# Performance work log

Hardware: AMD Instinct MI355X
Metric: run time of the kernel (lower is better)

## Reference

```python
import jax, jax.numpy as jnp
import numpy as np
import math

M = 0.5
S = 30.0
COS_M = math.cos(M)
SIN_M = math.sin(M)


def setup_inputs() -> dict:
    key = jax.random.key(0)
    k1, k2, k3 = jax.random.split(key, 3)
    batch, din, nclass = 512, 512, 100000
    x = jax.random.normal(k1, (batch, din), dtype=jnp.float32)
    # xavier_uniform for weight (out, in)
    limit = math.sqrt(6.0 / (nclass + din))
    w = jax.random.uniform(k2, (nclass, din), dtype=jnp.float32, minval=-limit, maxval=limit)
    target = jax.random.randint(k3, (batch,), 0, nclass, dtype=jnp.int64)
    return {"input": x, "weight": w, "target": target}


def reference(input, weight, target):
    # L2-normalize rows (torch F.normalize uses eps=1e-12 clamp on norm)
    xn = input / jnp.maximum(jnp.linalg.norm(input, axis=1, keepdims=True), 1e-12)
    wn = weight / jnp.maximum(jnp.linalg.norm(weight, axis=1, keepdims=True), 1e-12)
    cosine = xn @ wn.T  # [B, C]
    sine = jnp.sqrt(jnp.maximum(1.0 - cosine * cosine, 0.0))
    phi = cosine * COS_M - sine * SIN_M
    # easy_margin=True
    phi = jnp.where(cosine > 0, phi, cosine)
    one_hot = jax.nn.one_hot(target, cosine.shape[1], dtype=cosine.dtype)  # [B, C]
    logits = S * (one_hot * phi + (1.0 - one_hot) * cosine)
    # cross-entropy with mean reduction
    logp = jax.nn.log_softmax(logits, axis=1)
    nll = -jnp.take_along_axis(logp, target[:, None], axis=1)[:, 0]
    return jnp.mean(nll)
```

## Files before the change

### kernel.cpp

```cpp
#include <hip/hip_runtime.h>
#include <math.h>

#define BATCH 512
#define DIM 512
#define NCLASS 100000
#define BN 64
#define NBLK ((NCLASS + BN - 1) / BN)
#define S_SCALE 30.0f
#define COSM 0.8775825618903728f
#define SINM 0.4794255386042030f

typedef unsigned short u16;
typedef __attribute__((ext_vector_type(8))) short short8;
typedef __attribute__((ext_vector_type(4))) float floatx4;


__device__ __forceinline__ u16 f2bf(float f) {
    union { float f; unsigned int u; } v;
    v.f = f;
    unsigned int u = v.u;
    u += 0x7fffu + ((u >> 16) & 1u);
    return (u16)(u >> 16);
}

__global__ void xnorm_kernel(const float* __restrict__ x, u16* __restrict__ xn) {
    const int row = blockIdx.x;
    const int t = threadIdx.x;
    const floatx4* xr = (const floatx4*)(x + (size_t)row * DIM);
    floatx4 a = xr[t];
    floatx4 b = xr[t + 64];
    float ss = a[0]*a[0] + a[1]*a[1] + a[2]*a[2] + a[3]*a[3]
             + b[0]*b[0] + b[1]*b[1] + b[2]*b[2] + b[3]*b[3];
#pragma unroll
    for (int d = 1; d < 64; d <<= 1) ss += __shfl_xor(ss, d);
    const float rn = 1.0f / fmaxf(sqrtf(ss), 1e-12f);
    ushort4 ua, ub;
    ua.x = f2bf(a[0]*rn); ua.y = f2bf(a[1]*rn); ua.z = f2bf(a[2]*rn); ua.w = f2bf(a[3]*rn);
    ub.x = f2bf(b[0]*rn); ub.y = f2bf(b[1]*rn); ub.z = f2bf(b[2]*rn); ub.w = f2bf(b[3]*rn);
    u16* orow = xn + (size_t)row * DIM;
    *(ushort4*)(orow + 4*t)       = ua;
    *(ushort4*)(orow + 256 + 4*t) = ub;
}

__global__ void arcface_main(const float* __restrict__ w,
                             const u16* __restrict__ xn,
                             const int* __restrict__ target,
                             float* __restrict__ partials,
                             float* __restrict__ tlogit) {
    __shared__ u16 wb[BN * DIM];

    const int c0 = blockIdx.x * BN;
    const int t = threadIdx.x;

    {
        const int r = t >> 3;
        const int q = t & 7;
        const int cg = c0 + r;
        floatx4 v[16];
        float ss = 0.f;
        if (cg < NCLASS) {
            const floatx4* wr = (const floatx4*)(w + (size_t)cg * DIM);
#pragma unroll
            for (int i = 0; i < 16; ++i) {
                v[i] = wr[q + (i << 3)];
                ss += v[i][0]*v[i][0] + v[i][1]*v[i][1] + v[i][2]*v[i][2] + v[i][3]*v[i][3];
            }
        } else {
#pragma unroll
            for (int i = 0; i < 16; ++i) { v[i][0]=0.f; v[i][1]=0.f; v[i][2]=0.f; v[i][3]=0.f; }
        }
        ss += __shfl_xor(ss, 1);
        ss += __shfl_xor(ss, 2);
        ss += __shfl_xor(ss, 4);
        const float rs = 1.0f / fmaxf(sqrtf(ss), 1e-12f);
#pragma unroll
        for (int i = 0; i < 16; ++i) {
            const int col4 = q + (i << 3);
            const int gp = (col4 >> 1) ^ (r & 7);
            const int off = r * DIM + gp * 8 + (col4 & 1) * 4;
            ushort4 u;
            u.x = f2bf(v[i][0] * rs); u.y = f2bf(v[i][1] * rs);
            u.z = f2bf(v[i][2] * rs); u.w = f2bf(v[i][3] * rs);
            *(ushort4*)(&wb[off]) = u;
        }
    }
    __syncthreads();

    const int wave = t >> 6;
    const int lane = t & 63;
    const int quad = lane >> 4;
    const int nin  = lane & 15;
    const int mbase = wave * 64;

    floatx4 acc[4][4];
#pragma unroll
    for (int mi = 0; mi < 4; ++mi)
#pragma unroll
        for (int ni = 0; ni < 4; ++ni) {
            acc[mi][ni][0] = 0.f; acc[mi][ni][1] = 0.f;
            acc[mi][ni][2] = 0.f; acc[mi][ni][3] = 0.f;
        }

    for (int kk = 0; kk < 16; ++kk) {
        short8 a[4], b[4];
        const int k = kk * 32 + quad * 8;
#pragma unroll
        for (int mi = 0; mi < 4; ++mi) {
            const int m = mbase + mi * 16 + nin;
            a[mi] = *(const short8*)(xn + (size_t)m * DIM + k);
        }
#pragma unroll
        for (int ni = 0; ni < 4; ++ni) {
            const int cl = ni * 16 + nin;
            const int gp = ((kk << 2) + quad) ^ (cl & 7);
            b[ni] = *(const short8*)(&wb[cl * DIM + gp * 8]);
        }
#pragma unroll
        for (int mi = 0; mi < 4; ++mi)
#pragma unroll
            for (int ni = 0; ni < 4; ++ni)
                acc[mi][ni] = __builtin_amdgcn_mfma_f32_16x16x32_bf16(
                    a[mi], b[ni], acc[mi][ni], 0, 0, 0);
    }

#pragma unroll
    for (int mi = 0; mi < 4; ++mi) {
#pragma unroll
        for (int reg = 0; reg < 4; ++reg) {
            const int m = mbase + mi * 16 + quad * 4 + reg;
            const int tg = target[m];
            float psum = 0.f;
#pragma unroll
            for (int ni = 0; ni < 4; ++ni) {
                const int c = c0 + ni * 16 + nin;
                if (c < NCLASS) {
                    const float cosv = acc[mi][ni][reg];
                    float lg;
                    if (c == tg) {
                        const float sine = sqrtf(fmaxf(1.f - cosv * cosv, 0.f));
                        float phi = cosv * COSM - sine * SINM;
                        if (!(cosv > 0.f)) phi = cosv;
                        lg = S_SCALE * phi;
                        tlogit[m] = lg;
                    } else {
                        lg = S_SCALE * cosv;
                    }
                    psum += __expf(lg - S_SCALE);
                }
            }
            psum += __shfl_xor(psum, 1);
            psum += __shfl_xor(psum, 2);
            psum += __shfl_xor(psum, 4);
            psum += __shfl_xor(psum, 8);
            if (nin == 0)
                partials[(size_t)blockIdx.x * BATCH + m] = psum;
        }
    }
}

__global__ void reduce_lse(const float* __restrict__ partials,
                           const float* __restrict__ tlogit,
                           float* __restrict__ nll) {
    const int m = blockIdx.x;
    const int t = threadIdx.x;
    float s = 0.f;
    for (int b = t; b < NBLK; b += 256) s += partials[(size_t)b * BATCH + m];
#pragma unroll
    for (int d = 1; d < 64; d <<= 1) s += __shfl_xor(s, d);
    __shared__ float red[4];
    if ((t & 63) == 0) red[t >> 6] = s;
    __syncthreads();
    if (t == 0) {
        const float tot = red[0] + red[1] + red[2] + red[3];
        nll[m] = (logf(tot) + S_SCALE) - tlogit[m];
    }
}

__global__ void reduce_mean(const float* __restrict__ nll, float* __restrict__ out) {
    const int t = threadIdx.x;
    float s = nll[t];
#pragma unroll
    for (int d = 1; d < 64; d <<= 1) s += __shfl_xor(s, d);
    __shared__ float red[8];
    if ((t & 63) == 0) red[t >> 6] = s;
    __syncthreads();
    if (t == 0) {
        float tot = 0.f;
#pragma unroll
        for (int i = 0; i < 8; ++i) tot += red[i];
        out[0] = tot / (float)BATCH;
    }
}

extern "C" void kernel_launch(void* const* d_in, const int* in_sizes, int n_in,
                              void* d_out, int out_size, void* d_ws, size_t ws_size,
                              hipStream_t stream) {
    const float* x = (const float*)d_in[0];
    const float* w = (const float*)d_in[1];
    const int* target = (const int*)d_in[2];

    char* ws = (char*)d_ws;
    u16* xn        = (u16*)ws;
    float* tlogit  = (float*)(ws + 524288);
    float* nll     = (float*)(ws + 526336);
    float* partials= (float*)(ws + 528384);

    xnorm_kernel<<<BATCH, 64, 0, stream>>>(x, xn);
    arcface_main<<<NBLK, 512, 0, stream>>>(w, xn, target, partials, tlogit);
    reduce_lse<<<BATCH, 256, 0, stream>>>(partials, tlogit, nll);
    reduce_mean<<<1, 512, 0, stream>>>(nll, (float*)d_out);
}
```

Before: 402.4 us.

## Make main kernel persistent with double-buffered weight tiles and prefetch overlap

The main kernel now launches a fixed grid of 256 blocks that loop over class tiles. Each iteration loads the next tile's weights into registers during the MFMA loop and writes them into a second shared-memory buffer afterwards, so global loads overlap compute. The weight-norm scaling is applied to the accumulator instead of before bf16 conversion, targets are held in registers, and partials are stored row-major so the reduction reads contiguously. In exchange, register pressure is higher and LDS use doubles, which may limit occupancy, and rounding changes slightly because unnormalized weights are converted to bf16.

```diff
diff --git a/kernel.cpp b/kernel.cpp
--- a/kernel.cpp
+++ b/kernel.cpp
@@ -6,6 +6,7 @@
 #define NCLASS 100000
 #define BN 64
 #define NBLK ((NCLASS + BN - 1) / BN)
+#define GRID 256
 #define S_SCALE 30.0f
 #define COSM 0.8775825618903728f
 #define SINM 0.4794255386042030f
@@ -42,55 +43,43 @@
     *(ushort4*)(orow + 256 + 4*t) = ub;
 }
 
-__global__ void arcface_main(const float* __restrict__ w,
-                             const u16* __restrict__ xn,
-                             const int* __restrict__ target,
-                             float* __restrict__ partials,
-                             float* __restrict__ tlogit) {
-    __shared__ u16 wb[BN * DIM];
-
-    const int c0 = blockIdx.x * BN;
-    const int t = threadIdx.x;
-
-    {
-        const int r = t >> 3;
-        const int q = t & 7;
-        const int cg = c0 + r;
-        floatx4 v[16];
-        float ss = 0.f;
-        if (cg < NCLASS) {
-            const floatx4* wr = (const floatx4*)(w + (size_t)cg * DIM);
-#pragma unroll
-            for (int i = 0; i < 16; ++i) {
-                v[i] = wr[q + (i << 3)];
-                ss += v[i][0]*v[i][0] + v[i][1]*v[i][1] + v[i][2]*v[i][2] + v[i][3]*v[i][3];
-            }
-        } else {
-#pragma unroll
-            for (int i = 0; i < 16; ++i) { v[i][0]=0.f; v[i][1]=0.f; v[i][2]=0.f; v[i][3]=0.f; }
-        }
-        ss += __shfl_xor(ss, 1);
-        ss += __shfl_xor(ss, 2);
-        ss += __shfl_xor(ss, 4);
-        const float rs = 1.0f / fmaxf(sqrtf(ss), 1e-12f);
-#pragma unroll
-        for (int i = 0; i < 16; ++i) {
-            const int col4 = q + (i << 3);
-            const int gp = (col4 >> 1) ^ (r & 7);
-            const int off = r * DIM + gp * 8 + (col4 & 1) * 4;
-            ushort4 u;
-            u.x = f2bf(v[i][0] * rs); u.y = f2bf(v[i][1] * rs);
-            u.z = f2bf(v[i][2] * rs); u.w = f2bf(v[i][3] * rs);
-            *(ushort4*)(&wb[off]) = u;
-        }
-    }
-    __syncthreads();
-
-    const int wave = t >> 6;
-    const int lane = t & 63;
-    const int quad = lane >> 4;
-    const int nin  = lane & 15;
-    const int mbase = wave * 64;
+__device__ __forceinline__ void stage_write(const floatx4* v, u16* __restrict__ wbuf,
+                                            float* __restrict__ rsbuf, int sr, int sq) {
+    float ss = 0.f;
+#pragma unroll
+    for (int i = 0; i < 16; ++i)
+        ss += v[i][0]*v[i][0] + v[i][1]*v[i][1] + v[i][2]*v[i][2] + v[i][3]*v[i][3];
+    ss += __shfl_xor(ss, 1);
+    ss += __shfl_xor(ss, 2);
+    ss += __shfl_xor(ss, 4);
+    if (sq == 0) rsbuf[sr] = 1.0f / fmaxf(sqrtf(ss), 1e-12f);
+#pragma unroll
+    for (int i = 0; i < 16; ++i) {
+        const int col4 = sq + (i << 3);
+        const int gp = (col4 >> 1) ^ (sr & 7);
+        const int off = sr * DIM + gp * 8 + (col4 & 1) * 4;
+        ushort4 u;
+        u.x = f2bf(v[i][0]); u.y = f2bf(v[i][1]);
+        u.z = f2bf(v[i][2]); u.w = f2bf(v[i][3]);
+        *(ushort4*)(&wbuf[off]) = u;
+    }
+}
+
+template<bool PREF>
+__device__ __forceinline__ void process_tile(
+        const float* __restrict__ w, const u16* __restrict__ xn,
+        float* __restrict__ partials, float* __restrict__ tlogit,
+        const u16* __restrict__ wbc, u16* __restrict__ wbn,
+        const float* __restrict__ rsc, float* __restrict__ rsn,
+        const int* __restrict__ tgt, int tile,
+        int mbase, int quad, int nin, int sr, int sq) {
+
+    floatx4 v[16];
+    const floatx4* wr = (const floatx4*)w;
+    if (PREF) {
+        const int cg = min((tile + GRID) * BN + sr, NCLASS - 1);
+        wr = (const floatx4*)(w + (size_t)cg * DIM);
+    }
 
     floatx4 acc[4][4];
 #pragma unroll
@@ -101,19 +90,20 @@
             acc[mi][ni][2] = 0.f; acc[mi][ni][3] = 0.f;
         }
 
+    const u16* xbase = xn + (size_t)(mbase + nin) * DIM + quad * 8;
+
+#pragma unroll
     for (int kk = 0; kk < 16; ++kk) {
+        if (PREF) v[kk] = wr[sq + (kk << 3)];
         short8 a[4], b[4];
-        const int k = kk * 32 + quad * 8;
-#pragma unroll
-        for (int mi = 0; mi < 4; ++mi) {
-            const int m = mbase + mi * 16 + nin;
-            a[mi] = *(const short8*)(xn + (size_t)m * DIM + k);
-        }
+#pragma unroll
+        for (int mi = 0; mi < 4; ++mi)
+            a[mi] = *(const short8*)(xbase + (size_t)mi * 16 * DIM + kk * 32);
 #pragma unroll
         for (int ni = 0; ni < 4; ++ni) {
             const int cl = ni * 16 + nin;
             const int gp = ((kk << 2) + quad) ^ (cl & 7);
-            b[ni] = *(const short8*)(&wb[cl * DIM + gp * 8]);
+            b[ni] = *(const short8*)(&wbc[cl * DIM + gp * 8]);
         }
 #pragma unroll
         for (int mi = 0; mi < 4; ++mi)
@@ -123,18 +113,23 @@
                     a[mi], b[ni], acc[mi][ni], 0, 0, 0);
     }
 
+    const int c0 = tile * BN;
+    float rsl[4];
+#pragma unroll
+    for (int ni = 0; ni < 4; ++ni) rsl[ni] = rsc[ni * 16 + nin];
+
 #pragma unroll
     for (int mi = 0; mi < 4; ++mi) {
 #pragma unroll
         for (int reg = 0; reg < 4; ++reg) {
             const int m = mbase + mi * 16 + quad * 4 + reg;
-            const int tg = target[m];
+            const int tg = tgt[mi * 4 + reg];
             float psum = 0.f;
 #pragma unroll
             for (int ni = 0; ni < 4; ++ni) {
                 const int c = c0 + ni * 16 + nin;
                 if (c < NCLASS) {
-                    const float cosv = acc[mi][ni][reg];
+                    const float cosv = acc[mi][ni][reg] * rsl[ni];
                     float lg;
                     if (c == tg) {
                         const float sine = sqrtf(fmaxf(1.f - cosv * cosv, 0.f));
@@ -153,9 +148,59 @@
             psum += __shfl_xor(psum, 4);
             psum += __shfl_xor(psum, 8);
             if (nin == 0)
-                partials[(size_t)blockIdx.x * BATCH + m] = psum;
+                partials[(size_t)m * NBLK + tile] = psum;
         }
     }
+
+    if (PREF) stage_write(v, wbn, rsn, sr, sq);
+}
+
+__global__ __launch_bounds__(512, 2) void arcface_main(
+        const float* __restrict__ w, const u16* __restrict__ xn,
+        const int* __restrict__ target, float* __restrict__ partials,
+        float* __restrict__ tlogit) {
+    __shared__ __align__(16) u16 wb[2][BN * DIM];
+    __shared__ float rs_s[2][BN];
+
+    const int t = threadIdx.x;
+    const int wave = t >> 6;
+    const int lane = t & 63;
+    const int quad = lane >> 4;
+    const int nin  = lane & 15;
+    const int mbase = wave * 64;
+    const int sr = t >> 3;
+    const int sq = t & 7;
+
+    int tgt[16];
+#pragma unroll
+    for (int mi = 0; mi < 4; ++mi)
+#pragma unroll
+        for (int reg = 0; reg < 4; ++reg)
+            tgt[mi * 4 + reg] = target[mbase + mi * 16 + quad * 4 + reg];
+
+    {
+        const int cg = min((int)blockIdx.x * BN + sr, NCLASS - 1);
+        const floatx4* wr = (const floatx4*)(w + (size_t)cg * DIM);
+        floatx4 v[16];
+#pragma unroll
+        for (int i = 0; i < 16; ++i) v[i] = wr[sq + (i << 3)];
+        stage_write(v, wb[0], rs_s[0], sr, sq);
+    }
+    __syncthreads();
+
+    int cur = 0;
+    int tile = blockIdx.x;
+    while (tile + GRID < NBLK) {
+        process_tile<true>(w, xn, partials, tlogit,
+                           wb[cur], wb[cur ^ 1], rs_s[cur], rs_s[cur ^ 1],
+                           tgt, tile, mbase, quad, nin, sr, sq);
+        __syncthreads();
+        cur ^= 1;
+        tile += GRID;
+    }
+    process_tile<false>(w, xn, partials, tlogit,
+                        wb[cur], wb[cur ^ 1], rs_s[cur], rs_s[cur ^ 1],
+                        tgt, tile, mbase, quad, nin, sr, sq);
 }
 
 __global__ void reduce_lse(const float* __restrict__ partials,
@@ -163,8 +208,9 @@
                            float* __restrict__ nll) {
     const int m = blockIdx.x;
     const int t = threadIdx.x;
+    const float* row = partials + (size_t)m * NBLK;
     float s = 0.f;
-    for (int b = t; b < NBLK; b += 256) s += partials[(size_t)b * BATCH + m];
+    for (int b = t; b < NBLK; b += 256) s += row[b];
 #pragma unroll
     for (int d = 1; d < 64; d <<= 1) s += __shfl_xor(s, d);
     __shared__ float red[4];
@@ -206,7 +252,7 @@
     float* partials= (float*)(ws + 528384);
 
     xnorm_kernel<<<BATCH, 64, 0, stream>>>(x, xn);
-    arcface_main<<<NBLK, 512, 0, stream>>>(w, xn, target, partials, tlogit);
+    arcface_main<<<GRID, 512, 0, stream>>>(w, xn, target, partials, tlogit);
     reduce_lse<<<BATCH, 256, 0, stream>>>(partials, tlogit, nll);
     reduce_mean<<<1, 512, 0, stream>>>(nll, (float*)d_out);
 }
```

Result: slower. 573.6 us (+42.5%).

## Restructure ArcFace GEMM as persistent tiles with normalization folded into epilogue

Applied to the files above, without the earlier changes.

Replaces the one-block-per-64-classes kernel with a persistent 256-block grid. Each block holds a 128-row slice of normalized x in shared memory and streams 256-class weight tiles straight from global memory into registers. Weights are converted to bf16 in registers without normalizing, and the row norm is applied as a scale in the exp2 epilogue. The MFMA shape moves to 32x32x16. The target-logit margin is moved to reduce_lse, which recomputes the target cosine and swaps its exp term into the sum. This removes the shared-memory staging of W and shrinks the partials array, but adds recomputation and a dependency on reading x in bf16.

```diff
diff --git a/kernel.cpp b/kernel.cpp
--- a/kernel.cpp
+++ b/kernel.cpp
@@ -1,26 +1,34 @@
 #include <hip/hip_runtime.h>
+#include <hip/hip_bf16.h>
 #include <math.h>
 
 #define BATCH 512
 #define DIM 512
 #define NCLASS 100000
-#define BN 64
-#define NBLK ((NCLASS + BN - 1) / BN)
+#define BNB 256
+#define NT 391
+#define NSTREAM 64
+#define GRID 256
 #define S_SCALE 30.0f
 #define COSM 0.8775825618903728f
 #define SINM 0.4794255386042030f
+#define LOG2E 1.44269504088896f
 
 typedef unsigned short u16;
 typedef __attribute__((ext_vector_type(8))) short short8;
 typedef __attribute__((ext_vector_type(4))) float floatx4;
+typedef __attribute__((ext_vector_type(16))) float floatx16;
 
 
 __device__ __forceinline__ u16 f2bf(float f) {
+    union { __hip_bfloat16 h; u16 u; } c;
+    c.h = __float2bfloat16(f);
+    return c.u;
+}
+__device__ __forceinline__ float bf2f(u16 b) {
     union { float f; unsigned int u; } v;
-    v.f = f;
-    unsigned int u = v.u;
-    u += 0x7fffu + ((u >> 16) & 1u);
-    return (u16)(u >> 16);
+    v.u = ((unsigned int)b) << 16;
+    return v.f;
 }
 
 __global__ void xnorm_kernel(const float* __restrict__ x, u16* __restrict__ xn) {
@@ -42,137 +50,186 @@
     *(ushort4*)(orow + 256 + 4*t) = ub;
 }
 
-__global__ void arcface_main(const float* __restrict__ w,
-                             const u16* __restrict__ xn,
-                             const int* __restrict__ target,
-                             float* __restrict__ partials,
-                             float* __restrict__ tlogit) {
-    __shared__ u16 wb[BN * DIM];
-
-    const int c0 = blockIdx.x * BN;
-    const int t = threadIdx.x;
+__device__ __forceinline__ short8 cvt_bf8(floatx4 a, floatx4 b) {
+    union { short8 s8; u16 u[8]; } p;
+#pragma unroll
+    for (int j = 0; j < 4; ++j) p.u[j] = f2bf(a[j]);
+#pragma unroll
+    for (int j = 0; j < 4; ++j) p.u[4 + j] = f2bf(b[j]);
+    return p.s8;
+}
+
+__global__ __launch_bounds__(512, 1) void arcface_main(
+        const float* __restrict__ w, const u16* __restrict__ xn,
+        float* __restrict__ partials) {
+    __shared__ __align__(16) u16 ash[128 * 512];
+    __shared__ float pacc[8][64];
+
+    const int t = threadIdx.x;
+    const int bid = blockIdx.x;
+    const int stream = bid & 63;
+    const int mgrp = bid >> 6;
+    const int wv = t >> 6;
+    const int lane = t & 63;
+    const int l31 = lane & 31;
+    const int hi = lane >> 5;
+    const int mhalf = wv & 1;
+    const int nslot = wv >> 1;
 
     {
-        const int r = t >> 3;
-        const int q = t & 7;
-        const int cg = c0 + r;
-        floatx4 v[16];
-        float ss = 0.f;
-        if (cg < NCLASS) {
-            const floatx4* wr = (const floatx4*)(w + (size_t)cg * DIM);
-#pragma unroll
-            for (int i = 0; i < 16; ++i) {
-                v[i] = wr[q + (i << 3)];
-                ss += v[i][0]*v[i][0] + v[i][1]*v[i][1] + v[i][2]*v[i][2] + v[i][3]*v[i][3];
+        const u16* xbase = xn + (size_t)(mgrp * 128) * DIM;
+#pragma unroll
+        for (int i = 0; i < 16; ++i) {
+            const int gid = t + i * 512;
+            const int row = gid >> 6;
+            const int g = gid & 63;
+            floatx4 v = *(const floatx4*)(xbase + (size_t)row * DIM + g * 8);
+            *(floatx4*)(&ash[row * DIM + ((g ^ (row & 7)) * 8)]) = v;
+        }
+    }
+    __syncthreads();
+
+    float run[2][16];
+#pragma unroll
+    for (int mf = 0; mf < 2; ++mf)
+#pragma unroll
+        for (int r = 0; r < 16; ++r) run[mf][r] = 0.f;
+
+    const int arow0 = (mhalf * 64 + l31) * DIM;
+    const int arow1 = (mhalf * 64 + 32 + l31) * DIM;
+
+    for (int tile = stream; tile < NT; tile += NSTREAM) {
+        const int c0 = tile * BNB + nslot * 64;
+        bool vfrag[2];
+        const float* wp[2];
+#pragma unroll
+        for (int ni = 0; ni < 2; ++ni) {
+            const int c = c0 + ni * 32 + l31;
+            vfrag[ni] = (c0 + ni * 32) < NCLASS;
+            const int cc = min(c, NCLASS - 1);
+            wp[ni] = w + (size_t)cc * DIM + hi * 8;
+        }
+
+        floatx16 acc[2][2];
+#pragma unroll
+        for (int mf = 0; mf < 2; ++mf)
+#pragma unroll
+            for (int ni = 0; ni < 2; ++ni) acc[mf][ni] = (floatx16)0.0f;
+
+        float ssq[2] = {0.f, 0.f};
+        floatx4 pb[2][2][2];
+#pragma unroll
+        for (int ni = 0; ni < 2; ++ni) {
+            pb[0][ni][0] = *(const floatx4*)(wp[ni]);
+            pb[0][ni][1] = *(const floatx4*)(wp[ni] + 4);
+            pb[1][ni][0] = *(const floatx4*)(wp[ni] + 16);
+            pb[1][ni][1] = *(const floatx4*)(wp[ni] + 20);
+        }
+
+#pragma unroll
+        for (int ks = 0; ks < 32; ++ks) {
+            const int sl = ks & 1;
+            short8 bfr[2];
+#pragma unroll
+            for (int ni = 0; ni < 2; ++ni) {
+                floatx4 lo = pb[sl][ni][0], hp = pb[sl][ni][1];
+                ssq[ni] += lo[0]*lo[0] + lo[1]*lo[1] + lo[2]*lo[2] + lo[3]*lo[3]
+                         + hp[0]*hp[0] + hp[1]*hp[1] + hp[2]*hp[2] + hp[3]*hp[3];
+                bfr[ni] = cvt_bf8(lo, hp);
             }
-        } else {
-#pragma unroll
-            for (int i = 0; i < 16; ++i) { v[i][0]=0.f; v[i][1]=0.f; v[i][2]=0.f; v[i][3]=0.f; }
-        }
-        ss += __shfl_xor(ss, 1);
-        ss += __shfl_xor(ss, 2);
-        ss += __shfl_xor(ss, 4);
-        const float rs = 1.0f / fmaxf(sqrtf(ss), 1e-12f);
-#pragma unroll
-        for (int i = 0; i < 16; ++i) {
-            const int col4 = q + (i << 3);
-            const int gp = (col4 >> 1) ^ (r & 7);
-            const int off = r * DIM + gp * 8 + (col4 & 1) * 4;
-            ushort4 u;
-            u.x = f2bf(v[i][0] * rs); u.y = f2bf(v[i][1] * rs);
-            u.z = f2bf(v[i][2] * rs); u.w = f2bf(v[i][3] * rs);
-            *(ushort4*)(&wb[off]) = u;
-        }
-    }
-    __syncthreads();
-
-    const int wave = t >> 6;
-    const int lane = t & 63;
-    const int quad = lane >> 4;
-    const int nin  = lane & 15;
-    const int mbase = wave * 64;
-
-    floatx4 acc[4][4];
-#pragma unroll
-    for (int mi = 0; mi < 4; ++mi)
-#pragma unroll
-        for (int ni = 0; ni < 4; ++ni) {
-            acc[mi][ni][0] = 0.f; acc[mi][ni][1] = 0.f;
-            acc[mi][ni][2] = 0.f; acc[mi][ni][3] = 0.f;
-        }
-
-    for (int kk = 0; kk < 16; ++kk) {
-        short8 a[4], b[4];
-        const int k = kk * 32 + quad * 8;
-#pragma unroll
-        for (int mi = 0; mi < 4; ++mi) {
-            const int m = mbase + mi * 16 + nin;
-            a[mi] = *(const short8*)(xn + (size_t)m * DIM + k);
-        }
-#pragma unroll
-        for (int ni = 0; ni < 4; ++ni) {
-            const int cl = ni * 16 + nin;
-            const int gp = ((kk << 2) + quad) ^ (cl & 7);
-            b[ni] = *(const short8*)(&wb[cl * DIM + gp * 8]);
-        }
-#pragma unroll
-        for (int mi = 0; mi < 4; ++mi)
-#pragma unroll
-            for (int ni = 0; ni < 4; ++ni)
-                acc[mi][ni] = __builtin_amdgcn_mfma_f32_16x16x32_bf16(
-                    a[mi], b[ni], acc[mi][ni], 0, 0, 0);
-    }
-
-#pragma unroll
-    for (int mi = 0; mi < 4; ++mi) {
-#pragma unroll
-        for (int reg = 0; reg < 4; ++reg) {
-            const int m = mbase + mi * 16 + quad * 4 + reg;
-            const int tg = target[m];
-            float psum = 0.f;
-#pragma unroll
-            for (int ni = 0; ni < 4; ++ni) {
-                const int c = c0 + ni * 16 + nin;
-                if (c < NCLASS) {
-                    const float cosv = acc[mi][ni][reg];
-                    float lg;
-                    if (c == tg) {
-                        const float sine = sqrtf(fmaxf(1.f - cosv * cosv, 0.f));
-                        float phi = cosv * COSM - sine * SINM;
-                        if (!(cosv > 0.f)) phi = cosv;
-                        lg = S_SCALE * phi;
-                        tlogit[m] = lg;
-                    } else {
-                        lg = S_SCALE * cosv;
-                    }
-                    psum += __expf(lg - S_SCALE);
+            if (ks < 30) {
+#pragma unroll
+                for (int ni = 0; ni < 2; ++ni) {
+                    pb[sl][ni][0] = *(const floatx4*)(wp[ni] + (ks + 2) * 16);
+                    pb[sl][ni][1] = *(const floatx4*)(wp[ni] + (ks + 2) * 16 + 4);
                 }
             }
-            psum += __shfl_xor(psum, 1);
-            psum += __shfl_xor(psum, 2);
-            psum += __shfl_xor(psum, 4);
-            psum += __shfl_xor(psum, 8);
-            if (nin == 0)
-                partials[(size_t)blockIdx.x * BATCH + m] = psum;
-        }
+            const int gp = ((2 * ks + hi) ^ (l31 & 7)) * 8;
+            short8 a0 = *(const short8*)(&ash[arow0 + gp]);
+            short8 a1 = *(const short8*)(&ash[arow1 + gp]);
+            acc[0][0] = __builtin_amdgcn_mfma_f32_32x32x16_bf16(a0, bfr[0], acc[0][0], 0, 0, 0);
+            acc[0][1] = __builtin_amdgcn_mfma_f32_32x32x16_bf16(a0, bfr[1], acc[0][1], 0, 0, 0);
+            acc[1][0] = __builtin_amdgcn_mfma_f32_32x32x16_bf16(a1, bfr[0], acc[1][0], 0, 0, 0);
+            acc[1][1] = __builtin_amdgcn_mfma_f32_32x32x16_bf16(a1, bfr[1], acc[1][1], 0, 0, 0);
+        }
+
+        ssq[0] += __shfl_xor(ssq[0], 32);
+        ssq[1] += __shfl_xor(ssq[1], 32);
+#pragma unroll
+        for (int ni = 0; ni < 2; ++ni) {
+            if (!vfrag[ni]) continue;
+            const float sa = S_SCALE * (1.0f / fmaxf(sqrtf(ssq[ni]), 1e-12f)) * LOG2E;
+            const float sb = -S_SCALE * LOG2E;
+#pragma unroll
+            for (int mf = 0; mf < 2; ++mf)
+#pragma unroll
+                for (int r = 0; r < 16; ++r)
+                    run[mf][r] += exp2f(fmaf(acc[mf][ni][r], sa, sb));
+        }
+    }
+
+#pragma unroll
+    for (int mf = 0; mf < 2; ++mf)
+#pragma unroll
+        for (int r = 0; r < 16; ++r) {
+            float s = run[mf][r];
+            s += __shfl_xor(s, 1);
+            s += __shfl_xor(s, 2);
+            s += __shfl_xor(s, 4);
+            s += __shfl_xor(s, 8);
+            s += __shfl_xor(s, 16);
+            if (l31 == 0)
+                pacc[wv][mf * 32 + (r & 3) + 8 * (r >> 2) + 4 * hi] = s;
+        }
+    __syncthreads();
+    if (t < 128) {
+        const int h = t >> 6, r64 = t & 63;
+        const float s = pacc[h][r64] + pacc[h + 2][r64] + pacc[h + 4][r64] + pacc[h + 6][r64];
+        partials[(size_t)stream * BATCH + mgrp * 128 + t] = s;
     }
 }
 
 __global__ void reduce_lse(const float* __restrict__ partials,
-                           const float* __restrict__ tlogit,
+                           const float* __restrict__ w,
+                           const u16* __restrict__ xn,
+                           const int* __restrict__ target,
                            float* __restrict__ nll) {
     const int m = blockIdx.x;
     const int t = threadIdx.x;
-    float s = 0.f;
-    for (int b = t; b < NBLK; b += 256) s += partials[(size_t)b * BATCH + m];
-#pragma unroll
-    for (int d = 1; d < 64; d <<= 1) s += __shfl_xor(s, d);
-    __shared__ float red[4];
-    if ((t & 63) == 0) red[t >> 6] = s;
-    __syncthreads();
+    float tot = partials[(size_t)t * BATCH + m];
+#pragma unroll
+    for (int d = 1; d < 64; d <<= 1) tot += __shfl_xor(tot, d);
+
+    const int tg = target[m];
+    const float* wr = w + (size_t)tg * DIM + t * 8;
+    floatx4 w0 = *(const floatx4*)(wr);
+    floatx4 w1 = *(const floatx4*)(wr + 4);
+    short8 xv = *(const short8*)(xn + (size_t)m * DIM + t * 8);
+    float dot = 0.f, ssq = 0.f;
+#pragma unroll
+    for (int j = 0; j < 4; ++j) {
+        ssq += w0[j] * w0[j];
+        dot += bf2f((u16)xv[j]) * bf2f(f2bf(w0[j]));
+    }
+#pragma unroll
+    for (int j = 0; j < 4; ++j) {
+        ssq += w1[j] * w1[j];
+        dot += bf2f((u16)xv[4 + j]) * bf2f(f2bf(w1[j]));
+    }
+#pragma unroll
+    for (int d = 1; d < 64; d <<= 1) {
+        dot += __shfl_xor(dot, d);
+        ssq += __shfl_xor(ssq, d);
+    }
     if (t == 0) {
-        const float tot = red[0] + red[1] + red[2] + red[3];
-        nll[m] = (logf(tot) + S_SCALE) - tlogit[m];
+        const float rs = 1.0f / fmaxf(sqrtf(ssq), 1e-12f);
+        const float cosv = dot * rs;
+        const float sine = sqrtf(fmaxf(1.f - cosv * cosv, 0.f));
+        float phi = cosv * COSM - sine * SINM;
+        if (!(cosv > 0.f)) phi = cosv;
+        const float lgp = S_SCALE * phi, lgc = S_SCALE * cosv;
+        const float tt = tot - __expf(lgc - S_SCALE) + __expf(lgp - S_SCALE);
+        nll[m] = (logf(fmaxf(tt, 1e-30f)) + S_SCALE) - lgp;
     }
 }
 
@@ -201,12 +258,11 @@
 
     char* ws = (char*)d_ws;
     u16* xn        = (u16*)ws;
-    float* tlogit  = (float*)(ws + 524288);
-    float* nll     = (float*)(ws + 526336);
-    float* partials= (float*)(ws + 528384);
+    float* partials= (float*)(ws + 524288);
+    float* nll     = (float*)(ws + 655360);
 
     xnorm_kernel<<<BATCH, 64, 0, stream>>>(x, xn);
-    arcface_main<<<NBLK, 512, 0, stream>>>(w, xn, target, partials, tlogit);
-    reduce_lse<<<BATCH, 256, 0, stream>>>(partials, tlogit, nll);
+    arcface_main<<<GRID, 512, 0, stream>>>(w, xn, partials);
+    reduce_lse<<<BATCH, 64, 0, stream>>>(partials, w, xn, target, nll);
     reduce_mean<<<1, 512, 0, stream>>>(nll, (float*)d_out);
 }
```

New measurement: 531.3 us. +32.0%, slower.
